# Performance work log

Measured on AMD Instinct MI355X. Metric: run time of the kernel, lower is better.

## Reference

```python
import jax, jax.numpy as jnp
import numpy as np

SIZES = [4096, 12288, 20480, 20480, 8192]  # atoms of degree 0..4 (atoms sorted by degree)
N_ATOMS = sum(SIZES)
BATCH = 1024
N_TASKS, N_CLASSES = 12, 2
BN_EPS = 1e-3  # keras BatchNormalization default epsilon


def setup_inputs() -> dict:
    key = jax.random.key(0)
    ks = jax.random.split(key, 20)
    inp = {}
    inp["atom_features"] = jax.random.normal(ks[0], (N_ATOMS, 75), jnp.float32)
    starts = np.concatenate([[0], np.cumsum(SIZES)[:-1]])
    inp["degree_slice"] = jnp.asarray(np.stack([starts, np.array(SIZES)], 1), jnp.int32)
    inp["membership"] = jax.random.randint(ks[1], (N_ATOMS,), 0, BATCH, jnp.int32)
    inp["n_samples"] = BATCH
    for d in range(1, 5):
        inp[f"deg_adj_{d}"] = jax.random.randint(ks[1 + d], (SIZES[d], d), 0, N_ATOMS, jnp.int32)

    def w(k, shape, s=0.05):
        return s * jax.random.normal(k, shape, jnp.float32)

    # GraphConv weights: order [relW_deg1, selfW_deg1, ..., relW_deg4, selfW_deg4, selfW_deg0]
    inp["gc1_W"] = w(ks[6], (9, 75, 256)); inp["gc1_b"] = w(ks[7], (9, 256))
    inp["gc2_W"] = w(ks[8], (9, 256, 256)); inp["gc2_b"] = w(ks[9], (9, 256))

    def bn_params(k, c):  # rows: gamma, beta, moving_mean, moving_var
        g = 1.0 + 0.1 * jax.random.normal(k, (c,), jnp.float32)
        b = 0.1 * jax.random.normal(jax.random.fold_in(k, 1), (c,), jnp.float32)
        return jnp.stack([g, b, jnp.zeros((c,), jnp.float32), jnp.ones((c,), jnp.float32)])

    inp["bn1"] = bn_params(ks[10], 256)
    inp["bn2"] = bn_params(ks[11], 256)
    inp["bn3"] = bn_params(ks[12], 512)
    inp["dense_W"] = w(ks[13], (256, 512)); inp["dense_b"] = w(ks[14], (512,))
    inp["head_W"] = w(ks[15], (2 * 512, N_TASKS * N_CLASSES)); inp["head_b"] = w(ks[16], (N_TASKS * N_CLASSES,))
    return inp


def _graph_conv(x, adjs, W, b):
    # degree-0 atoms: self transform only (last weight matrix)
    pieces = [x[: SIZES[0]] @ W[8] + b[8]]
    off = SIZES[0]
    for d in range(1, 5):
        nd = SIZES[d]
        self_atoms = x[off: off + nd]
        rel = jnp.take(x, adjs[d - 1], axis=0).sum(axis=1)  # [nd, F] neighbor sum
        out = rel @ W[2 * (d - 1)] + b[2 * (d - 1)] + self_atoms @ W[2 * d - 1] + b[2 * d - 1]
        pieces.append(out)
        off += nd
    return jax.nn.relu(jnp.concatenate(pieces, axis=0))


def _graph_pool(x, adjs):
    pieces = [x[: SIZES[0]]]  # degree-0: passthrough
    off = SIZES[0]
    for d in range(1, 5):
        nd = SIZES[d]
        self_atoms = x[off: off + nd]
        neigh = jnp.take(x, adjs[d - 1], axis=0)  # [nd, d, F]
        pieces.append(jnp.maximum(self_atoms, neigh.max(axis=1)))
        off += nd
    return jnp.concatenate(pieces, axis=0)


def _bn(x, p):  # inference batchnorm with moving stats
    g, b, m, v = p
    return g * (x - m) * jax.lax.rsqrt(v + BN_EPS) + b


def reference(atom_features, degree_slice, membership, n_samples,
              deg_adj_1, deg_adj_2, deg_adj_3, deg_adj_4,
              gc1_W, gc1_b, gc2_W, gc2_b, bn1, bn2, bn3,
              dense_W, dense_b, head_W, head_b):
    adjs = (deg_adj_1, deg_adj_2, deg_adj_3, deg_adj_4)
    x = atom_features
    for W, b, bn in ((gc1_W, gc1_b, bn1), (gc2_W, gc2_b, bn2)):
        x = _bn(_graph_conv(x, adjs, W, b), bn)
        x = _graph_pool(x, adjs)
    h = _bn(jax.nn.relu(x @ dense_W + dense_b), bn3)  # [N_ATOMS, 512]
    # GraphGather: per-molecule sum and max, tanh activation
    seg_sum = jax.ops.segment_sum(h, membership, num_segments=BATCH)
    seg_max = jax.ops.segment_max(h, membership, num_segments=BATCH)
    fp = jnp.tanh(jnp.concatenate([seg_sum, seg_max], axis=1))  # neural fingerprint [BATCH, 1024]
    logits = (fp @ head_W + head_b).reshape(BATCH, N_TASKS, N_CLASSES)[: int(n_samples)]  # trim
    return jax.nn.softmax(logits, axis=-1), logits, fp
```

## Files before the change

### kernel.cpp

```cpp
#include <hip/hip_runtime.h>
#include <hip/hip_bf16.h>
#include <math.h>

#define NA 65536
#define MAXSEG 160

typedef _Float16 half8 __attribute__((ext_vector_type(8)));
typedef _Float16 h4    __attribute__((ext_vector_type(4)));
typedef float float4v  __attribute__((ext_vector_type(4)));


__device__ __forceinline__ void atom_seg(int atom, int& d, int& loc,
                                         const int* a1, const int* a2,
                                         const int* a3, const int* a4,
                                         const int*& adj) {
    if (atom < 4096)       { d = 0; loc = 0; adj = nullptr; }
    else if (atom < 16384) { d = 1; adj = a1; loc = atom - 4096; }
    else if (atom < 36864) { d = 2; adj = a2; loc = atom - 16384; }
    else if (atom < 57344) { d = 3; adj = a3; loc = atom - 36864; }
    else                   { d = 4; adj = a4; loc = atom - 57344; }
}

__global__ void zero_count_kernel(int* __restrict__ count) {
    int i = blockIdx.x * 256 + threadIdx.x;
    if (i < 1024) count[i] = 0;
}

__global__ void bucket_kernel(const int* __restrict__ mem, int* __restrict__ count,
                              int* __restrict__ list) {
    int i = blockIdx.x * 256 + threadIdx.x;
    int seg = mem[i];
    int pos = atomicAdd(&count[seg], 1);
    if (pos < MAXSEG) list[seg * MAXSEG + pos] = i;
}

__global__ void cvt_w1_kernel(const float* __restrict__ gc1W, const float* __restrict__ gc1b,
                              _Float16* __restrict__ Wc1, float* __restrict__ bias1) {
    int idx = blockIdx.x * 256 + threadIdx.x;
    if (idx < 204800) {
        int k = idx % 160, n = (idx / 160) & 255, seg = idx / (160 * 256);
        float v = 0.f;
        if (k < 75) { int w = (seg == 0) ? 8 : (2 * seg - 1); v = gc1W[(w * 75 + k) * 256 + n]; }
        else if (k < 150 && seg > 0) { int w = 2 * (seg - 1); v = gc1W[(w * 75 + (k - 75)) * 256 + n]; }
        Wc1[(size_t)(seg * 256 + n) * 160 + k] = (_Float16)v;
    }
    if (idx < 1280) {
        int n = idx & 255, seg = idx >> 8;
        bias1[idx] = (seg == 0) ? gc1b[8 * 256 + n]
                                : gc1b[(2 * seg - 1) * 256 + n] + gc1b[2 * (seg - 1) * 256 + n];
    }
}

__global__ void cvt_w2_kernel(const float* __restrict__ gc2W, const float* __restrict__ gc2b,
                              _Float16* __restrict__ Wc2, float* __restrict__ bias2) {
    int idx = blockIdx.x * 256 + threadIdx.x;
    if (idx < 655360) {
        int k = idx & 511, n = (idx >> 9) & 255, seg = idx >> 17;
        float v = 0.f;
        if (k < 256) { int w = (seg == 0) ? 8 : (2 * seg - 1); v = gc2W[(w * 256 + k) * 256 + n]; }
        else if (seg > 0) { int w = 2 * (seg - 1); v = gc2W[(w * 256 + (k - 256)) * 256 + n]; }
        Wc2[(size_t)(seg * 256 + n) * 512 + k] = (_Float16)v;
    }
    if (idx < 1280) {
        int n = idx & 255, seg = idx >> 8;
        bias2[idx] = (seg == 0) ? gc2b[8 * 256 + n]
                                : gc2b[(2 * seg - 1) * 256 + n] + gc2b[2 * (seg - 1) * 256 + n];
    }
}

__global__ void cvt_wd_kernel(const float* __restrict__ dW, _Float16* __restrict__ dWt) {
    int idx = blockIdx.x * 256 + threadIdx.x;
    int n = idx >> 8, k = idx & 255;
    dWt[(size_t)n * 256 + k] = (_Float16)dW[(size_t)k * 512 + n];
}

__global__ void cvt_hw_kernel(const float* __restrict__ hW, float* __restrict__ hWt) {
    int idx = blockIdx.x * 256 + threadIdx.x;
    int o = idx / 1024, k = idx & 1023;
    hWt[idx] = hW[k * 24 + o];
}

__global__ __launch_bounds__(256) void gather1_kernel(
    const float* __restrict__ af,
    const int* __restrict__ a1, const int* __restrict__ a2,
    const int* __restrict__ a3, const int* __restrict__ a4,
    _Float16* __restrict__ X1) {
    int atom = blockIdx.x * 4 + (threadIdx.x >> 6);
    int lane = threadIdx.x & 63;
    int d, loc; const int* adj;
    atom_seg(atom, d, loc, a1, a2, a3, a4, adj);
    int nb[4];
    for (int j = 0; j < d; j++) nb[j] = adj[(size_t)loc * d + j];
    for (int k = lane; k < 75; k += 64) {
        X1[(size_t)atom * 160 + k] = (_Float16)af[(size_t)atom * 75 + k];
        float s = 0.f;
        for (int j = 0; j < d; j++) s += af[(size_t)nb[j] * 75 + k];
        X1[(size_t)atom * 160 + 75 + k] = (_Float16)s;
    }
    if (lane < 10) X1[(size_t)atom * 160 + 150 + lane] = (_Float16)0.f;
}

__global__ __launch_bounds__(256) void gather2_kernel(
    const _Float16* __restrict__ p,
    const int* __restrict__ a1, const int* __restrict__ a2,
    const int* __restrict__ a3, const int* __restrict__ a4,
    _Float16* __restrict__ X2) {
    int atom = blockIdx.x * 4 + (threadIdx.x >> 6);
    int lane = threadIdx.x & 63;
    int d, loc; const int* adj;
    atom_seg(atom, d, loc, a1, a2, a3, a4, adj);
    int nb[4];
    for (int j = 0; j < d; j++) nb[j] = adj[(size_t)loc * d + j];
    h4 self = *(const h4*)(p + (size_t)atom * 256 + lane * 4);
    *(h4*)(X2 + (size_t)atom * 512 + lane * 4) = self;
    float s0 = 0.f, s1 = 0.f, s2 = 0.f, s3 = 0.f;
    for (int j = 0; j < d; j++) {
        h4 v = *(const h4*)(p + (size_t)nb[j] * 256 + lane * 4);
        s0 += (float)v[0]; s1 += (float)v[1]; s2 += (float)v[2]; s3 += (float)v[3];
    }
    h4 o; o[0] = (_Float16)s0; o[1] = (_Float16)s1; o[2] = (_Float16)s2; o[3] = (_Float16)s3;
    *(h4*)(X2 + (size_t)atom * 512 + 256 + lane * 4) = o;
}

template<int K, int N>
__global__ __launch_bounds__(256) void gemm_kernel(
    const _Float16* __restrict__ X, const _Float16* __restrict__ Wt,
    const float* __restrict__ bias, const float* __restrict__ bnp,
    int wstride, int bstride, _Float16* __restrict__ out) {
    __shared__ _Float16 As[128 * 40];
    __shared__ _Float16 Bs[128 * 40];
    int m0 = blockIdx.x * 128, n0 = blockIdx.y * 128;
    int t = m0 >> 7;
    int seg = (t < 32) ? 0 : (t < 128) ? 1 : (t < 288) ? 2 : (t < 448) ? 3 : 4;
    const _Float16* Wb = Wt + (size_t)seg * wstride;
    const float* bia = bias + seg * bstride;
    int tid = threadIdx.x, lane = tid & 63, wave = tid >> 6;
    int wm = (wave >> 1) * 64, wn = (wave & 1) * 64;
    int lrow = lane & 15, lq = lane >> 4;
    float4v acc[4][4] = {};
    for (int kc = 0; kc < K / 32; kc++) {
        #pragma unroll
        for (int p = tid; p < 512; p += 256) {
            int row = p >> 2, cch = p & 3;
            *(uint4*)(As + row * 40 + cch * 8) =
                *(const uint4*)(X + (size_t)(m0 + row) * K + kc * 32 + cch * 8);
            *(uint4*)(Bs + row * 40 + cch * 8) =
                *(const uint4*)(Wb + (size_t)(n0 + row) * K + kc * 32 + cch * 8);
        }
        __syncthreads();
        half8 af[4], bf[4];
        #pragma unroll
        for (int i = 0; i < 4; i++) {
            af[i] = *(const half8*)(As + (wm + i * 16 + lrow) * 40 + lq * 8);
            bf[i] = *(const half8*)(Bs + (wn + i * 16 + lrow) * 40 + lq * 8);
        }
        #pragma unroll
        for (int mi = 0; mi < 4; mi++)
            #pragma unroll
            for (int ni = 0; ni < 4; ni++)
                acc[mi][ni] = __builtin_amdgcn_mfma_f32_16x16x32_f16(af[mi], bf[ni], acc[mi][ni], 0, 0, 0);
        __syncthreads();
    }
    #pragma unroll
    for (int ni = 0; ni < 4; ni++) {
        int col = n0 + wn + ni * 16 + lrow;
        float bv = bia[col], g = bnp[col], be = bnp[N + col];
        float mn = bnp[2 * N + col], vr = bnp[3 * N + col];
        float sc = g * rsqrtf(vr + 1e-3f);
        #pragma unroll
        for (int mi = 0; mi < 4; mi++) {
            int rbase = m0 + wm + mi * 16 + lq * 4;
            #pragma unroll
            for (int r = 0; r < 4; r++) {
                float v = acc[mi][ni][r] + bv;
                v = fmaxf(v, 0.f);
                v = sc * (v - mn) + be;
                out[(size_t)(rbase + r) * N + col] = (_Float16)v;
            }
        }
    }
}

__global__ __launch_bounds__(256) void pool_f16_kernel(
    const _Float16* __restrict__ x,
    const int* __restrict__ a1, const int* __restrict__ a2,
    const int* __restrict__ a3, const int* __restrict__ a4,
    _Float16* __restrict__ out) {
    int atom = blockIdx.x * 4 + (threadIdx.x >> 6);
    int lane = threadIdx.x & 63;
    int d, loc; const int* adj;
    atom_seg(atom, d, loc, a1, a2, a3, a4, adj);
    h4 m = *(const h4*)(x + (size_t)atom * 256 + lane * 4);
    float m0 = (float)m[0], m1 = (float)m[1], m2 = (float)m[2], m3 = (float)m[3];
    for (int j = 0; j < d; j++) {
        int nb = adj[(size_t)loc * d + j];
        h4 v = *(const h4*)(x + (size_t)nb * 256 + lane * 4);
        m0 = fmaxf(m0, (float)v[0]); m1 = fmaxf(m1, (float)v[1]);
        m2 = fmaxf(m2, (float)v[2]); m3 = fmaxf(m3, (float)v[3]);
    }
    h4 o; o[0] = (_Float16)m0; o[1] = (_Float16)m1; o[2] = (_Float16)m2; o[3] = (_Float16)m3;
    *(h4*)(out + (size_t)atom * 256 + lane * 4) = o;
}

__global__ __launch_bounds__(512) void seg_reduce_kernel(
    const _Float16* __restrict__ h, const int* __restrict__ count,
    const int* __restrict__ list, float* __restrict__ fp) {
    int seg = blockIdx.x, c = threadIdx.x;
    int n = count[seg]; if (n > MAXSEG) n = MAXSEG;
    float sum = 0.f, mx = -INFINITY;
    for (int a = 0; a < n; a++) {
        int row = list[seg * MAXSEG + a];
        float v = (float)h[(size_t)row * 512 + c];
        sum += v; mx = fmaxf(mx, v);
    }
    fp[(size_t)seg * 1024 + c] = tanhf(sum);
    fp[(size_t)seg * 1024 + 512 + c] = tanhf(mx);
}

__global__ __launch_bounds__(256) void head_kernel(
    const float* __restrict__ fp, const float* __restrict__ hWt,
    const float* __restrict__ hb, float* __restrict__ logits,
    float* __restrict__ probs) {
    __shared__ float fps[1024];
    __shared__ float red[32];
    int s = blockIdx.x;
    for (int i = threadIdx.x; i < 1024; i += 256) fps[i] = fp[(size_t)s * 1024 + i];
    __syncthreads();
    int t = threadIdx.x;
    int o = t >> 3, kp = t & 7;
    float acc = 0.f;
    if (o < 24) {
        const float* w = hWt + (size_t)o * 1024 + kp * 128;
        const float* f = fps + kp * 128;
        #pragma unroll 8
        for (int i = 0; i < 128; i++) acc = fmaf(f[i], w[i], acc);
    }
    acc += __shfl_down(acc, 4, 64);
    acc += __shfl_down(acc, 2, 64);
    acc += __shfl_down(acc, 1, 64);
    if (o < 24 && kp == 0) red[o] = acc + hb[o];
    __syncthreads();
    if (t < 24) {
        float a = red[t];
        float an = red[t ^ 1];
        logits[(size_t)s * 24 + t] = a;
        probs[(size_t)s * 24 + t] = 1.f / (1.f + expf(an - a));
    }
}

extern "C" void kernel_launch(void* const* d_in, const int* in_sizes, int n_in,
                              void* d_out, int out_size, void* d_ws, size_t ws_size,
                              hipStream_t stream) {
    const float* af         = (const float*)d_in[0];
    const int*   membership = (const int*)d_in[2];
    const int*   a1 = (const int*)d_in[4];
    const int*   a2 = (const int*)d_in[5];
    const int*   a3 = (const int*)d_in[6];
    const int*   a4 = (const int*)d_in[7];
    const float* gc1W = (const float*)d_in[8];
    const float* gc1b = (const float*)d_in[9];
    const float* gc2W = (const float*)d_in[10];
    const float* gc2b = (const float*)d_in[11];
    const float* bn1  = (const float*)d_in[12];
    const float* bn2  = (const float*)d_in[13];
    const float* bn3  = (const float*)d_in[14];
    const float* dW   = (const float*)d_in[15];
    const float* db   = (const float*)d_in[16];
    const float* hW   = (const float*)d_in[17];
    const float* hb   = (const float*)d_in[18];

    float* out    = (float*)d_out;
    float* probs  = out;
    float* logits = out + 24576;
    float* fp     = out + 49152;

    _Float16* Wc1  = (_Float16*)d_ws;
    _Float16* Wc2  = Wc1 + 204800;
    _Float16* dWt  = Wc2 + 655360;
    float* bias1   = (float*)(dWt + 131072);
    float* bias2   = bias1 + 1280;
    float* hWt     = bias2 + 1280;
    int* count     = (int*)(hWt + 24576);
    int* list      = count + 1024;
    _Float16* bufBig = (_Float16*)(list + 163840);
    _Float16* bufY   = bufBig + (size_t)NA * 512;
    _Float16* bufP   = bufY + (size_t)NA * 256;

    zero_count_kernel<<<4, 256, 0, stream>>>(count);
    bucket_kernel<<<256, 256, 0, stream>>>(membership, count, list);
    cvt_w1_kernel<<<800, 256, 0, stream>>>(gc1W, gc1b, Wc1, bias1);
    cvt_w2_kernel<<<2560, 256, 0, stream>>>(gc2W, gc2b, Wc2, bias2);
    cvt_wd_kernel<<<512, 256, 0, stream>>>(dW, dWt);
    cvt_hw_kernel<<<96, 256, 0, stream>>>(hW, hWt);

    gather1_kernel<<<16384, 256, 0, stream>>>(af, a1, a2, a3, a4, bufBig);
    gemm_kernel<160, 256><<<dim3(512, 2), 256, 0, stream>>>(bufBig, Wc1, bias1, bn1,
                                                            256 * 160, 256, bufY);
    pool_f16_kernel<<<16384, 256, 0, stream>>>(bufY, a1, a2, a3, a4, bufP);
    gather2_kernel<<<16384, 256, 0, stream>>>(bufP, a1, a2, a3, a4, bufBig);
    gemm_kernel<512, 256><<<dim3(512, 2), 256, 0, stream>>>(bufBig, Wc2, bias2, bn2,
                                                            256 * 512, 256, bufY);
    pool_f16_kernel<<<16384, 256, 0, stream>>>(bufY, a1, a2, a3, a4, bufP);
    gemm_kernel<256, 512><<<dim3(512, 4), 256, 0, stream>>>(bufP, dWt, db, bn3,
                                                            0, 0, bufBig);
    seg_reduce_kernel<<<1024, 512, 0, stream>>>(bufBig, count, list, fp);
    head_kernel<<<1024, 256, 0, stream>>>(fp, hWt, hb, logits, probs);
}
```

Before: 378.9 us.

## Skip self-feature copy in gather2, widen GEMM K tile with XOR-swizzled LDS

gather2 now writes only the neighbor sums into a separate buffer. The second GEMM reads the self half of its K dimension straight from the pooled buffer, which removes a 256-column copy per atom. The GEMM kernel gains a template BK (64 for the K=512 and K=256 GEMMs), an XOR-swizzled LDS layout in place of the padded stride, and a 1D grid with N-blocks adjacent. The aim is fewer barriers per K, fewer LDS bank conflicts and better L2 reuse of A tiles, at the cost of more LDS per block and a per-chunk source-pointer branch.

```diff
diff --git a/kernel.cpp b/kernel.cpp
--- a/kernel.cpp
+++ b/kernel.cpp
@@ -100,36 +100,38 @@
     if (lane < 10) X1[(size_t)atom * 160 + 150 + lane] = (_Float16)0.f;
 }
 
-__global__ __launch_bounds__(256) void gather2_kernel(
+__global__ __launch_bounds__(256) void gather2n_kernel(
     const _Float16* __restrict__ p,
     const int* __restrict__ a1, const int* __restrict__ a2,
     const int* __restrict__ a3, const int* __restrict__ a4,
-    _Float16* __restrict__ X2) {
+    _Float16* __restrict__ Xn) {
     int atom = blockIdx.x * 4 + (threadIdx.x >> 6);
     int lane = threadIdx.x & 63;
     int d, loc; const int* adj;
     atom_seg(atom, d, loc, a1, a2, a3, a4, adj);
     int nb[4];
     for (int j = 0; j < d; j++) nb[j] = adj[(size_t)loc * d + j];
-    h4 self = *(const h4*)(p + (size_t)atom * 256 + lane * 4);
-    *(h4*)(X2 + (size_t)atom * 512 + lane * 4) = self;
     float s0 = 0.f, s1 = 0.f, s2 = 0.f, s3 = 0.f;
     for (int j = 0; j < d; j++) {
         h4 v = *(const h4*)(p + (size_t)nb[j] * 256 + lane * 4);
         s0 += (float)v[0]; s1 += (float)v[1]; s2 += (float)v[2]; s3 += (float)v[3];
     }
     h4 o; o[0] = (_Float16)s0; o[1] = (_Float16)s1; o[2] = (_Float16)s2; o[3] = (_Float16)s3;
-    *(h4*)(X2 + (size_t)atom * 512 + 256 + lane * 4) = o;
-}
-
-template<int K, int N>
+    *(h4*)(Xn + (size_t)atom * 256 + lane * 4) = o;
+}
+
+template<int K, int N, int BK, int SPLIT>
 __global__ __launch_bounds__(256) void gemm_kernel(
-    const _Float16* __restrict__ X, const _Float16* __restrict__ Wt,
+    const _Float16* __restrict__ X, const _Float16* __restrict__ Xn,
+    const _Float16* __restrict__ Wt,
     const float* __restrict__ bias, const float* __restrict__ bnp,
     int wstride, int bstride, _Float16* __restrict__ out) {
-    __shared__ _Float16 As[128 * 40];
-    __shared__ _Float16 Bs[128 * 40];
-    int m0 = blockIdx.x * 128, n0 = blockIdx.y * 128;
+    constexpr int NC8 = BK / 8;
+    __shared__ _Float16 As[128 * BK];
+    __shared__ _Float16 Bs[128 * BK];
+    constexpr int nb = N / 128;
+    int bid = blockIdx.x;
+    int m0 = (bid / nb) * 128, n0 = (bid % nb) * 128;
     int t = m0 >> 7;
     int seg = (t < 32) ? 0 : (t < 128) ? 1 : (t < 288) ? 2 : (t < 448) ? 3 : 4;
     const _Float16* Wb = Wt + (size_t)seg * wstride;
@@ -138,27 +140,42 @@
     int wm = (wave >> 1) * 64, wn = (wave & 1) * 64;
     int lrow = lane & 15, lq = lane >> 4;
     float4v acc[4][4] = {};
-    for (int kc = 0; kc < K / 32; kc++) {
+    for (int kc = 0; kc < K / BK; kc++) {
         #pragma unroll
-        for (int p = tid; p < 512; p += 256) {
-            int row = p >> 2, cch = p & 3;
-            *(uint4*)(As + row * 40 + cch * 8) =
-                *(const uint4*)(X + (size_t)(m0 + row) * K + kc * 32 + cch * 8);
-            *(uint4*)(Bs + row * 40 + cch * 8) =
-                *(const uint4*)(Wb + (size_t)(n0 + row) * K + kc * 32 + cch * 8);
+        for (int p = tid; p < 128 * NC8; p += 256) {
+            int row = p / NC8, c8 = p % NC8;
+            int cs = c8 ^ (row & (NC8 - 1));
+            const _Float16* srcA;
+            if (!SPLIT) {
+                srcA = X + (size_t)(m0 + row) * K + kc * BK + c8 * 8;
+            } else {
+                int kcol = kc * BK + c8 * 8;
+                srcA = (kcol < 256) ? X  + (size_t)(m0 + row) * 256 + kcol
+                                    : Xn + (size_t)(m0 + row) * 256 + (kcol - 256);
+            }
+            *(uint4*)(As + row * BK + cs * 8) = *(const uint4*)srcA;
+            *(uint4*)(Bs + row * BK + cs * 8) =
+                *(const uint4*)(Wb + (size_t)(n0 + row) * K + kc * BK + c8 * 8);
         }
         __syncthreads();
-        half8 af[4], bf[4];
         #pragma unroll
-        for (int i = 0; i < 4; i++) {
-            af[i] = *(const half8*)(As + (wm + i * 16 + lrow) * 40 + lq * 8);
-            bf[i] = *(const half8*)(Bs + (wn + i * 16 + lrow) * 40 + lq * 8);
+        for (int kl = 0; kl < BK / 32; kl++) {
+            half8 af[4], bf[4];
+            #pragma unroll
+            for (int i = 0; i < 4; i++) {
+                int ra = wm + i * 16 + lrow;
+                int ca = (kl * 4 + lq) ^ (ra & (NC8 - 1));
+                af[i] = *(const half8*)(As + ra * BK + ca * 8);
+                int rb = wn + i * 16 + lrow;
+                int cb = (kl * 4 + lq) ^ (rb & (NC8 - 1));
+                bf[i] = *(const half8*)(Bs + rb * BK + cb * 8);
+            }
+            #pragma unroll
+            for (int mi = 0; mi < 4; mi++)
+                #pragma unroll
+                for (int ni = 0; ni < 4; ni++)
+                    acc[mi][ni] = __builtin_amdgcn_mfma_f32_16x16x32_f16(af[mi], bf[ni], acc[mi][ni], 0, 0, 0);
         }
-        #pragma unroll
-        for (int mi = 0; mi < 4; mi++)
-            #pragma unroll
-            for (int ni = 0; ni < 4; ni++)
-                acc[mi][ni] = __builtin_amdgcn_mfma_f32_16x16x32_f16(af[mi], bf[ni], acc[mi][ni], 0, 0, 0);
         __syncthreads();
     }
     #pragma unroll
@@ -285,6 +302,9 @@
     _Float16* bufBig = (_Float16*)(list + 163840);
     _Float16* bufY   = bufBig + (size_t)NA * 512;
     _Float16* bufP   = bufY + (size_t)NA * 256;
+    _Float16* X1 = bufBig;
+    _Float16* Xn = bufBig + (size_t)NA * 256;
+    _Float16* h  = bufBig;
 
     zero_count_kernel<<<4, 256, 0, stream>>>(count);
     bucket_kernel<<<256, 256, 0, stream>>>(membership, count, list);
@@ -293,16 +313,16 @@
     cvt_wd_kernel<<<512, 256, 0, stream>>>(dW, dWt);
     cvt_hw_kernel<<<96, 256, 0, stream>>>(hW, hWt);
 
-    gather1_kernel<<<16384, 256, 0, stream>>>(af, a1, a2, a3, a4, bufBig);
-    gemm_kernel<160, 256><<<dim3(512, 2), 256, 0, stream>>>(bufBig, Wc1, bias1, bn1,
-                                                            256 * 160, 256, bufY);
+    gather1_kernel<<<16384, 256, 0, stream>>>(af, a1, a2, a3, a4, X1);
+    gemm_kernel<160, 256, 32, 0><<<1024, 256, 0, stream>>>(X1, nullptr, Wc1, bias1, bn1,
+                                                           256 * 160, 256, bufY);
     pool_f16_kernel<<<16384, 256, 0, stream>>>(bufY, a1, a2, a3, a4, bufP);
-    gather2_kernel<<<16384, 256, 0, stream>>>(bufP, a1, a2, a3, a4, bufBig);
-    gemm_kernel<512, 256><<<dim3(512, 2), 256, 0, stream>>>(bufBig, Wc2, bias2, bn2,
-                                                            256 * 512, 256, bufY);
+    gather2n_kernel<<<16384, 256, 0, stream>>>(bufP, a1, a2, a3, a4, Xn);
+    gemm_kernel<512, 256, 64, 1><<<1024, 256, 0, stream>>>(bufP, Xn, Wc2, bias2, bn2,
+                                                           256 * 512, 256, bufY);
     pool_f16_kernel<<<16384, 256, 0, stream>>>(bufY, a1, a2, a3, a4, bufP);
-    gemm_kernel<256, 512><<<dim3(512, 4), 256, 0, stream>>>(bufP, dWt, db, bn3,
-                                                            0, 0, bufBig);
-    seg_reduce_kernel<<<1024, 512, 0, stream>>>(bufBig, count, list, fp);
+    gemm_kernel<256, 512, 64, 0><<<2048, 256, 0, stream>>>(bufP, nullptr, dWt, db, bn3,
+                                                           0, 0, h);
+    seg_reduce_kernel<<<1024, 512, 0, stream>>>(h, count, list, fp);
     head_kernel<<<1024, 256, 0, stream>>>(fp, hWt, hb, logits, probs);
 }
```

Result: faster. 368.7 us (-2.7%).
